# Performance work log

Hardware: AMD Instinct MI355X
Metric: run time of the kernel (lower is better)

Reference implementation:

```python
import jax, jax.numpy as jnp
import numpy as np

N = 100000      # nodes
E = 1600000     # edges (avg degree 16)
IN = 128
OUT = 256


def setup_inputs() -> dict:
    key = jax.random.key(0)
    ks = jax.random.split(key, 8)
    x = jax.random.normal(ks[0], (N, IN), dtype=jnp.float32)
    edge_index = jax.random.randint(ks[1], (2, E), 0, N, dtype=jnp.int64)
    # GCNConv weights (glorot-ish scale) and biases
    W1 = jax.random.normal(ks[2], (IN, OUT), dtype=jnp.float32) / np.float32(np.sqrt(IN))
    b1 = jnp.zeros((OUT,), jnp.float32)
    W2 = jax.random.normal(ks[3], (OUT, OUT), dtype=jnp.float32) / np.float32(np.sqrt(OUT))
    b2 = jnp.zeros((OUT,), jnp.float32)
    # projection Linear(IN, OUT)
    Wp = jax.random.normal(ks[4], (IN, OUT), dtype=jnp.float32) / np.float32(np.sqrt(IN))
    bp = jax.random.normal(ks[5], (OUT,), dtype=jnp.float32) * 0.01
    return {"x": x, "edge_index": edge_index, "W1": W1, "b1": b1,
            "W2": W2, "b2": b2, "Wp": Wp, "bp": bp}


def _gcn_conv(x, W, b, src, dst, n):
    """PyG GCNConv: D^{-1/2}(A+I)D^{-1/2} X W + b. src/dst already include self-loops."""
    xw = x @ W                                              # [n, out]
    ones = jnp.ones(src.shape[0], dtype=xw.dtype)
    deg = jax.ops.segment_sum(ones, dst, num_segments=n)    # in-degree incl. self-loop
    dinv = jnp.where(deg > 0, jax.lax.rsqrt(deg), 0.0)
    norm = dinv[src] * dinv[dst]                            # [e]
    msgs = xw[src] * norm[:, None]                          # gather + scale
    out = jax.ops.segment_sum(msgs, dst, num_segments=n)    # scatter-add
    return out + b


def reference(x, edge_index, W1, b1, W2, b2, Wp, bp):
    n = x.shape[0]
    loop = jnp.arange(n, dtype=edge_index.dtype)            # self-loops
    src = jnp.concatenate([edge_index[0], loop])
    dst = jnp.concatenate([edge_index[1], loop])
    out = jax.nn.relu(_gcn_conv(x, W1, b1, src, dst, n))
    out = _gcn_conv(out, W2, b2, src, dst, n)
    identity = x @ Wp + bp                                  # projection (IN != OUT)
    return jax.nn.relu(out + identity)
```

## Files before the change

### kernel.cpp

```cpp
#include <hip/hip_runtime.h>

#define NODES 100000
#define EDGES 1600000
#define FIN   128
#define FOUT  256
#define NBUCK 196
#define NBLKS 98

typedef __bf16 bf16;
typedef __bf16 bf16x8 __attribute__((ext_vector_type(8)));
typedef __bf16 bf16x4 __attribute__((ext_vector_type(4)));
typedef __bf16 bf16x2 __attribute__((ext_vector_type(2)));
typedef float  f32x4  __attribute__((ext_vector_type(4)));
typedef float  f32x2  __attribute__((ext_vector_type(2)));

__device__ __forceinline__ f32x2 bf2f(unsigned w) {
    f32x2 r;
    r[0] = __uint_as_float(w << 16);
    r[1] = __uint_as_float(w & 0xffff0000u);
    return r;
}

__device__ __forceinline__ void acc_u4(f32x2 a[4], uint4 w) {
    a[0] += bf2f(w.x); a[1] += bf2f(w.y);
    a[2] += bf2f(w.z); a[3] += bf2f(w.w);
}

__device__ __forceinline__ int edge_at(const int* __restrict__ ei, int which, int i,
                                       int is64) {
    if (is64) return ei[2 * (which * EDGES + i)];
    return ei[which * EDGES + i];
}

__global__ __launch_bounds__(256) void init_kernel(const void* __restrict__ x,
                                                   const int* __restrict__ ei,
                                                   int* __restrict__ zero0,
                                                   int* __restrict__ flags,
                                                   float* __restrict__ zpadA,
                                                   float* __restrict__ zpadB) {
    int b = blockIdx.x, t = threadIdx.x;
    if (b < 394) {
        int i = b * 256 + t;
        if (i < 100864) zero0[i] = 0;
        return;
    }
    zpadA[t] = 0.0f;
    zpadB[t] = 0.0f;
    __shared__ int s_f32_evidence;
    __shared__ int s_odd_nonzero;
    if (t == 0) { s_f32_evidence = 0; s_odd_nonzero = 0; }
    __syncthreads();
    const bf16* xb = (const bf16*)x;
    int local_f32 = 0;
    for (int i = t; i < 4096; i += 256) {
        float v = fabsf((float)xb[i]);
        if (!(v < 1e4f)) local_f32 = 1;
    }
    if (local_f32) atomicOr(&s_f32_evidence, 1);
    int local_odd = 0;
    for (int k = t; k < 1024; k += 256) {
        if (ei[2 * k + 1] != 0) local_odd = 1;
    }
    if (local_odd) atomicOr(&s_odd_nonzero, 1);
    __syncthreads();
    if (t == 0) {
        flags[0] = s_f32_evidence ? 0 : 1;
        flags[1] = s_odd_nonzero ? 0 : 1;
    }
}

__global__ __launch_bounds__(512) void degcnt_pack(const int* __restrict__ ei,
                                                   int* __restrict__ deg,
                                                   int* __restrict__ bhist,
                                                   const void* __restrict__ W1,
                                                   const void* __restrict__ W2,
                                                   const void* __restrict__ Wp,
                                                   const void* __restrict__ b1,
                                                   const void* __restrict__ b2,
                                                   const void* __restrict__ bp,
                                                   bf16* __restrict__ W1p, bf16* __restrict__ W2p,
                                                   bf16* __restrict__ Wpp, bf16* __restrict__ b1b,
                                                   bf16* __restrict__ b2b, bf16* __restrict__ bpb,
                                                   const int* __restrict__ flags) {
    if (blockIdx.x < 3125) {
        __shared__ int lh[256];
        int t = threadIdx.x;
        if (t < 256) lh[t] = 0;
        __syncthreads();
        int i = blockIdx.x * 512 + t;
        if (i < EDGES) {
            int is64 = flags[1];
            int s = edge_at(ei, 0, i, is64);
            int d = edge_at(ei, 1, i, is64);
            if (s >= 0 && s < NODES && d >= 0 && d < NODES) {
                atomicAdd(&deg[d], 1);
                atomicAdd(&lh[d >> 9], 1);
            }
        }
        __syncthreads();
        if (t < NBUCK && lh[t] > 0) atomicAdd(&bhist[t], lh[t]);
        return;
    }
    if (threadIdx.x >= 256) return;
    int fl = flags[0];
    int b = blockIdx.x - 3125;
    if (b < 512) {
        const void* W; bf16* Wo; int idx;
        if (b < 128)      { W = W1; Wo = W1p; idx = b * 256 + threadIdx.x; }
        else if (b < 384) { W = W2; Wo = W2p; idx = (b - 128) * 256 + threadIdx.x; }
        else              { W = Wp; Wo = Wpp; idx = (b - 384) * 256 + threadIdx.x; }
        int j    = idx & 7;
        int lane = (idx >> 3) & 63;
        int ct   = (idx >> 9) & 15;
        int kt   = idx >> 13;
        int k = kt * 32 + (lane >> 4) * 8 + j;
        int n = ct * 16 + (lane & 15);
        Wo[idx] = fl ? ((const bf16*)W)[k * 256 + n]
                     : (bf16)(((const float*)W)[k * 256 + n]);
    } else {
        const void* bb; bf16* bo;
        if (b == 512)      { bb = b1; bo = b1b; }
        else if (b == 513) { bb = b2; bo = b2b; }
        else               { bb = bp; bo = bpb; }
        int i = threadIdx.x;
        bo[i] = fl ? ((const bf16*)bb)[i] : (bf16)(((const float*)bb)[i]);
    }
}

__global__ __launch_bounds__(1024) void scan1(const int* __restrict__ deg,
                                              int* __restrict__ col_ptr,
                                              int* __restrict__ blksum, int n) {
    __shared__ int sm[1024];
    int t = threadIdx.x;
    int i = blockIdx.x * 1024 + t;
    int v = (i < n) ? deg[i] + 1 : 0;
    sm[t] = v;
    __syncthreads();
    for (int off = 1; off < 1024; off <<= 1) {
        int u = (t >= off) ? sm[t - off] : 0;
        __syncthreads();
        sm[t] += u;
        __syncthreads();
    }
    if (i <= n) col_ptr[i] = sm[t] - v;
    if (t == 1023) blksum[blockIdx.x] = sm[t];
}

#define EPB 4096
__global__ __launch_bounds__(256) void part_scan3(const int* __restrict__ ei,
                                                  const int* __restrict__ bhist,
                                                  int* __restrict__ bcur,
                                                  uint2* __restrict__ pairs,
                                                  const int* __restrict__ flags,
                                                  int* __restrict__ col_ptr,
                                                  const int* __restrict__ blk,
                                                  const int* __restrict__ deg,
                                                  float* __restrict__ dinv,
                                                  int* __restrict__ col_idx, int n) {
    if (blockIdx.x < 391) {
        __shared__ int lh[256], sc[256], lst[256], lcu[256], gb[256], bs[256];
        __shared__ uint2 stage[EPB];
        int t = threadIdx.x;
        int base = blockIdx.x * EPB;
        int is64 = flags[1];

        lh[t] = 0;
        __syncthreads();

        int es[16], ed[16];
#pragma unroll
        for (int j = 0; j < 16; ++j) {
            int i = base + j * 256 + t;
            int s = -1, d = -1;
            if (i < EDGES) {
                s = edge_at(ei, 0, i, is64);
                d = edge_at(ei, 1, i, is64);
                if (s < 0 || s >= NODES || d < 0 || d >= NODES) d = -1;
            }
            es[j] = s; ed[j] = d;
            if (d >= 0) atomicAdd(&lh[d >> 9], 1);
        }
        __syncthreads();
        sc[t] = lh[t];
        __syncthreads();
        for (int off = 1; off < 256; off <<= 1) {
            int u = (t >= off) ? sc[t - off] : 0;
            __syncthreads();
            sc[t] += u;
            __syncthreads();
        }
        int start = sc[t] - lh[t];
        lst[t] = start;
        lcu[t] = start;
        __syncthreads();
#pragma unroll
        for (int j = 0; j < 16; ++j) {
            if (ed[j] >= 0) {
                int p = atomicAdd(&lcu[ed[j] >> 9], 1);
                stage[p] = make_uint2((unsigned)es[j], (unsigned)ed[j]);
            }
        }
        __syncthreads();
        int v2 = (t < NBUCK) ? bhist[t] : 0;
        bs[t] = v2;
        __syncthreads();
        for (int off = 1; off < 256; off <<= 1) {
            int u = (t >= off) ? bs[t - off] : 0;
            __syncthreads();
            bs[t] += u;
            __syncthreads();
        }
        if (t < NBUCK && lh[t] > 0)
            gb[t] = (bs[t] - v2) + atomicAdd(&bcur[t], lh[t]);
        __syncthreads();
        int nval = sc[255];
        for (int slot = t; slot < nval; slot += 256) {
            uint2 e = stage[slot];
            int b = (int)(e.y >> 9);
            pairs[(size_t)gb[b] + (slot - lst[b])] = e;
        }
        return;
    }
    __shared__ int sb[128];
    int t = threadIdx.x;
    int sid = blockIdx.x - 391;
    int ov = 0;
    if (t < 128) { ov = (t < NBLKS) ? blk[t] : 0; sb[t] = ov; }
    __syncthreads();
    for (int off = 1; off < 128; off <<= 1) {
        int u = (t >= off && t < 128) ? sb[t - off] : 0;
        __syncthreads();
        if (t < 128) sb[t] += u;
        __syncthreads();
    }
    if (t < 128) sb[t] -= ov;
    __syncthreads();
    int i = sid * 256 + t;
    if (i <= n) {
        int v = col_ptr[i] + sb[i >> 10];
        col_ptr[i] = v;
        if (i < n) col_idx[v] = i;
    }
    if (i < n) dinv[i] = rsqrtf((float)deg[i] + 1.0f);
}

__global__ __launch_bounds__(256) void ff_proj(const uint2* __restrict__ pairs,
                                               const int* __restrict__ bhist,
                                               const int* __restrict__ col_ptr,
                                               int* __restrict__ col_idx,
                                               const void* __restrict__ Av,
                                               const bf16* __restrict__ Wpk,
                                               const float* __restrict__ dinv,
                                               const bf16* __restrict__ biasp,
                                               const bf16* __restrict__ bias2,
                                               void* __restrict__ outv,
                                               bf16* __restrict__ projb,
                                               int use_projb,
                                               bf16* __restrict__ Xs,
                                               const int* __restrict__ flags) {
    if (blockIdx.x < NBUCK) {
        __shared__ int lcur[512];
        __shared__ int bs2[256];
        int b = blockIdx.x;
        int t = threadIdx.x;
        int v2 = (t < NBUCK) ? bhist[t] : 0;
        bs2[t] = v2;
        __syncthreads();
        for (int off = 1; off < 256; off <<= 1) {
            int u = (t >= off) ? bs2[t - off] : 0;
            __syncthreads();
            bs2[t] += u;
            __syncthreads();
        }
        int be = bs2[b];
        int bb = be - bhist[b];
        int node = (b << 9) + t;
        lcur[t] = (node < NODES) ? col_ptr[node] + 1 : 0;
        int node2 = node + 256;
        lcur[t + 256] = (node2 < NODES) ? col_ptr[node2] + 1 : 0;
        __syncthreads();
        for (int i = bb + t; i < be; i += 256) {
            uint2 e = pairs[i];
            int pos = atomicAdd(&lcur[e.y & 511], 1);
            col_idx[pos] = (int)e.x;
        }
        return;
    }
    int a_f32 = (flags[0] == 0);
    int wave = threadIdx.x >> 6;
    int lane = threadIdx.x & 63;
    int row0 = (blockIdx.x - NBUCK) * 64;
    int lr = lane & 15;
    int lk = (lane >> 4) * 8;

    int arow[4];
    float di4[4];
#pragma unroll
    for (int rf = 0; rf < 4; ++rf) {
        int r = row0 + rf * 16 + lr;
        arow[rf] = r < NODES ? r : (NODES - 1);
        di4[rf] = dinv[arow[rf]];
    }

    f32x4 acc[4][4];
    f32x4 z = {0.f, 0.f, 0.f, 0.f};
#pragma unroll
    for (int i = 0; i < 4; ++i)
#pragma unroll
        for (int j = 0; j < 4; ++j) acc[i][j] = z;

    for (int kt = 0; kt < 4; ++kt) {
        bf16x8 af[4];
        if (!a_f32) {
            const bf16* Ab = (const bf16*)Av + kt * 32 + lk;
#pragma unroll
            for (int rf = 0; rf < 4; ++rf)
                af[rf] = *(const bf16x8*)(Ab + (size_t)arow[rf] * FIN);
        } else {
            const float* Af = (const float*)Av + kt * 32 + lk;
#pragma unroll
            for (int rf = 0; rf < 4; ++rf) {
                const float* p = Af + (size_t)arow[rf] * FIN;
                f32x4 lo = *(const f32x4*)p;
                f32x4 hi = *(const f32x4*)(p + 4);
                af[rf][0] = (bf16)lo[0]; af[rf][1] = (bf16)lo[1];
                af[rf][2] = (bf16)lo[2]; af[rf][3] = (bf16)lo[3];
                af[rf][4] = (bf16)hi[0]; af[rf][5] = (bf16)hi[1];
                af[rf][6] = (bf16)hi[2]; af[rf][7] = (bf16)hi[3];
            }
        }
#pragma unroll
        for (int rf = 0; rf < 4; ++rf) {
            bf16x8 xsv;
#pragma unroll
            for (int j = 0; j < 8; ++j) xsv[j] = (bf16)(di4[rf] * (float)af[rf][j]);
            *(bf16x8*)(Xs + (size_t)arow[rf] * FIN + kt * 32 + lk) = xsv;
        }
        const bf16* wb = Wpk + ((size_t)(kt * 16 + wave * 4) * 64 + lane) * 8;
        bf16x8 bfv[4];
#pragma unroll
        for (int cf = 0; cf < 4; ++cf)
            bfv[cf] = *(const bf16x8*)(wb + cf * 512);
#pragma unroll
        for (int rf = 0; rf < 4; ++rf)
#pragma unroll
            for (int cf = 0; cf < 4; ++cf)
                acc[rf][cf] = __builtin_amdgcn_mfma_f32_16x16x32_bf16(
                    af[rf], bfv[cf], acc[rf][cf], 0, 0, 0);
    }

    int rb = (lane >> 4) * 4;
#pragma unroll
    for (int rf = 0; rf < 4; ++rf) {
#pragma unroll
        for (int r = 0; r < 4; ++r) {
            int row = row0 + rf * 16 + rb + r;
            if (row >= NODES) continue;
#pragma unroll
            for (int cf = 0; cf < 4; ++cf) {
                int col = wave * 64 + cf * 16 + lr;
                float v = acc[rf][cf][r] + (float)biasp[col] + (float)bias2[col];
                size_t off = (size_t)row * 256 + col;
                if (a_f32) {
                    if (use_projb) projb[off] = (bf16)v;
                    else           ((float*)outv)[off] = v;
                } else {
                    ((bf16*)outv)[off] = (bf16)v;
                }
            }
        }
    }
}

__device__ __forceinline__ f32x2 sel_reduce4(f32x2 a[4], int rg) {
    f32x2 k0 = (rg & 2) ? a[2] : a[0];
    f32x2 k1 = (rg & 2) ? a[3] : a[1];
    f32x2 s0 = (rg & 2) ? a[0] : a[2];
    f32x2 s1 = (rg & 2) ? a[1] : a[3];
    f32x2 t;
    t[0] = __shfl_xor(s0[0], 32); t[1] = __shfl_xor(s0[1], 32); k0 += t;
    t[0] = __shfl_xor(s1[0], 32); t[1] = __shfl_xor(s1[1], 32); k1 += t;
    f32x2 c = (rg & 1) ? k1 : k0;
    f32x2 s = (rg & 1) ? k0 : k1;
    t[0] = __shfl_xor(s[0], 16); t[1] = __shfl_xor(s[1], 16); c += t;
    return c;
}

#define SMLD 264
__global__ __launch_bounds__(512) void g1conv(const int* __restrict__ col_ptr,
                                              const int* __restrict__ col_idx,
                                              const bf16* __restrict__ Xs,
                                              const float* __restrict__ dinv,
                                              const bf16* __restrict__ W1p,
                                              const bf16* __restrict__ W2p,
                                              const bf16* __restrict__ b1b,
                                              bf16* __restrict__ Y2) {
    __shared__ bf16 sm[64][SMLD];
    int wave = threadIdx.x >> 6;
    int lane = threadIdx.x & 63;
    int row0 = blockIdx.x * 64;
    int li = lane & 15;
    int rg = lane >> 4;

    const char* Xl = (const char*)Xs + li * 16;
    for (int k = 0; k < 8; ++k) {
        int node = row0 + wave * 8 + k;
        int nn = node < NODES ? node : (NODES - 1);
        int beg = col_ptr[nn], end = col_ptr[nn + 1];
        float di = dinv[nn];
        f32x2 a[4];
#pragma unroll
        for (int d = 0; d < 4; ++d) { a[d][0] = 0.f; a[d][1] = 0.f; }
        for (int chunk = beg; chunk < end; chunk += 64) {
            int gpos = chunk + lane;
            int idx = -2;
            if (gpos < end) idx = col_idx[gpos];
            int moff = idx << 8;
            int cnt = end - chunk; if (cnt > 64) cnt = 64;
            int j = 0;
            for (; j + 16 <= cnt; j += 16) {
                int so0 = __shfl(moff, j + rg);
                int so1 = __shfl(moff, j + 4 + rg);
                int so2 = __shfl(moff, j + 8 + rg);
                int so3 = __shfl(moff, j + 12 + rg);
                uint4 w0 = *(const uint4*)(Xl + so0);
                uint4 w1 = *(const uint4*)(Xl + so1);
                uint4 w2 = *(const uint4*)(Xl + so2);
                uint4 w3 = *(const uint4*)(Xl + so3);
                acc_u4(a, w0); acc_u4(a, w1);
                acc_u4(a, w2); acc_u4(a, w3);
            }
            for (; j < cnt; j += 4) {
                int so = __shfl(moff, j + rg);
                uint4 w = *(const uint4*)(Xl + so);
                acc_u4(a, w);
            }
        }
        f32x2 s = sel_reduce4(a, rg);
        bf16x2 o;
        o[0] = (bf16)(di * s[0]);
        o[1] = (bf16)(di * s[1]);
        *(bf16x2*)&sm[wave * 8 + k][li * 8 + rg * 2] = o;
    }
    __syncthreads();

    int wr = wave & 1;
    int wc = wave >> 1;
    int lr = li;
    int lk = rg * 8;
    f32x4 acc[2][4];
    f32x4 z = {0.f, 0.f, 0.f, 0.f};
#pragma unroll
    for (int i = 0; i < 2; ++i)
#pragma unroll
        for (int j = 0; j < 4; ++j) acc[i][j] = z;
    for (int kt = 0; kt < 4; ++kt) {
        bf16x8 af[2];
#pragma unroll
        for (int rf = 0; rf < 2; ++rf)
            af[rf] = *(const bf16x8*)&sm[wr * 32 + rf * 16 + lr][kt * 32 + lk];
        const bf16* wb = W1p + ((size_t)(kt * 16 + wc * 4) * 64 + lane) * 8;
        bf16x8 bfv[4];
#pragma unroll
        for (int cf = 0; cf < 4; ++cf)
            bfv[cf] = *(const bf16x8*)(wb + cf * 512);
#pragma unroll
        for (int rf = 0; rf < 2; ++rf)
#pragma unroll
            for (int cf = 0; cf < 4; ++cf)
                acc[rf][cf] = __builtin_amdgcn_mfma_f32_16x16x32_bf16(
                    af[rf], bfv[cf], acc[rf][cf], 0, 0, 0);
    }
    __syncthreads();

    int rb = rg * 4;
#pragma unroll
    for (int rf = 0; rf < 2; ++rf)
#pragma unroll
        for (int r = 0; r < 4; ++r) {
            int row = wr * 32 + rf * 16 + rb + r;
#pragma unroll
            for (int cf = 0; cf < 4; ++cf) {
                int col = wc * 64 + cf * 16 + lr;
                float v = acc[rf][cf][r] + (float)b1b[col];
                sm[row][col] = (bf16)fmaxf(v, 0.0f);
            }
        }
    __syncthreads();

#pragma unroll
    for (int i = 0; i < 2; ++i)
#pragma unroll
        for (int j = 0; j < 4; ++j) acc[i][j] = z;
    for (int kt = 0; kt < 8; ++kt) {
        bf16x8 af[2];
#pragma unroll
        for (int rf = 0; rf < 2; ++rf)
            af[rf] = *(const bf16x8*)&sm[wr * 32 + rf * 16 + lr][kt * 32 + lk];
        const bf16* wb = W2p + ((size_t)(kt * 16 + wc * 4) * 64 + lane) * 8;
        bf16x8 bfv[4];
#pragma unroll
        for (int cf = 0; cf < 4; ++cf)
            bfv[cf] = *(const bf16x8*)(wb + cf * 512);
#pragma unroll
        for (int rf = 0; rf < 2; ++rf)
#pragma unroll
            for (int cf = 0; cf < 4; ++cf)
                acc[rf][cf] = __builtin_amdgcn_mfma_f32_16x16x32_bf16(
                    af[rf], bfv[cf], acc[rf][cf], 0, 0, 0);
    }
#pragma unroll
    for (int rf = 0; rf < 2; ++rf)
#pragma unroll
        for (int r = 0; r < 4; ++r) {
            int row = row0 + wr * 32 + rf * 16 + rb + r;
            if (row >= NODES) continue;
            float di = dinv[row];
#pragma unroll
            for (int cf = 0; cf < 4; ++cf) {
                int col = wc * 64 + cf * 16 + lr;
                Y2[(size_t)row * 256 + col] = (bf16)(acc[rf][cf][r] * di);
            }
        }
}

__global__ __launch_bounds__(256) void gather2(const int* __restrict__ col_ptr,
                                               const int* __restrict__ col_idx,
                                               const bf16* __restrict__ Y2,
                                               const float* __restrict__ dinv,
                                               const bf16* __restrict__ projb,
                                               int use_projb,
                                               void* __restrict__ outv,
                                               const int* __restrict__ flags) {
    int io_f32 = (flags[0] == 0);
    int b = blockIdx.x;
    int slice = b & 1;
    int wave  = threadIdx.x >> 6;
    int wid   = (b >> 1) * 4 + wave;
    int lane  = threadIdx.x & 63;
    if (wid >= NODES) return;
    int beg = col_ptr[wid], end = col_ptr[wid + 1];
    int li = lane & 15;
    int rg = lane >> 4;
    int ch0 = slice * 128 + li * 8 + rg * 2;
    size_t obase = (size_t)wid * 256 + ch0;

    float di = dinv[wid];
    float pj0, pj1;
    if (io_f32) {
        if (use_projb) {
            bf16x2 p = *(const bf16x2*)(projb + obase);
            pj0 = (float)p[0]; pj1 = (float)p[1];
        } else {
            f32x2 p = *(const f32x2*)((const float*)outv + obase);
            pj0 = p[0]; pj1 = p[1];
        }
    } else {
        bf16x2 p = *(const bf16x2*)((const bf16*)outv + obase);
        pj0 = (float)p[0]; pj1 = (float)p[1];
    }

    const char* Yl = (const char*)Y2 + slice * 256 + li * 16;
    f32x2 acc2[4];
#pragma unroll
    for (int d = 0; d < 4; ++d) { acc2[d][0] = 0.f; acc2[d][1] = 0.f; }
    for (int chunk = beg; chunk < end; chunk += 64) {
        int gpos = chunk + lane;
        int idx = -2;
        if (gpos < end) idx = col_idx[gpos];
        int moff = idx << 9;
        int cnt = end - chunk; if (cnt > 64) cnt = 64;
        int j = 0;
        for (; j + 16 <= cnt; j += 16) {
            int so0 = __shfl(moff, j + rg);
            int so1 = __shfl(moff, j + 4 + rg);
            int so2 = __shfl(moff, j + 8 + rg);
            int so3 = __shfl(moff, j + 12 + rg);
            uint4 w0 = *(const uint4*)(Yl + so0);
            uint4 w1 = *(const uint4*)(Yl + so1);
            uint4 w2 = *(const uint4*)(Yl + so2);
            uint4 w3 = *(const uint4*)(Yl + so3);
            acc_u4(acc2, w0); acc_u4(acc2, w1);
            acc_u4(acc2, w2); acc_u4(acc2, w3);
        }
        for (; j < cnt; j += 4) {
            int so = __shfl(moff, j + rg);
            uint4 w = *(const uint4*)(Yl + so);
            acc_u4(acc2, w);
        }
    }
    f32x2 s = sel_reduce4(acc2, rg);
    float r0 = fmaxf(di * s[0] + pj0, 0.0f);
    float r1 = fmaxf(di * s[1] + pj1, 0.0f);

    if (io_f32) {
        f32x2 o; o[0] = r0; o[1] = r1;
        __builtin_nontemporal_store(o, (f32x2*)((float*)outv + obase));
    } else {
        bf16x2 o; o[0] = (bf16)r0; o[1] = (bf16)r1;
        __builtin_nontemporal_store(o, (bf16x2*)((bf16*)outv + obase));
    }
}

__global__ __launch_bounds__(256) void zero_out(bf16* out, int nelem) {
    int i = blockIdx.x * 256 + threadIdx.x;
    if (i < nelem) out[i] = (bf16)0.0f;
}

extern "C" void kernel_launch(void* const* d_in, const int* in_sizes, int n_in,
                              void* d_out, int out_size, void* d_ws, size_t ws_size,
                              hipStream_t stream) {
    const void* x   = d_in[0];
    const int*  ei  = (const int*)d_in[1];
    const void* W1  = d_in[2];
    const void* b1  = d_in[3];
    const void* W2  = d_in[4];
    const void* b2  = d_in[5];
    const void* Wp  = d_in[6];
    const void* bp  = d_in[7];

    const size_t CIDX_ALLOC = 6800384;
    const size_t NEEDED     = 85074432;
    const size_t NEEDED_BIG = NEEDED + 51200000;
    if (ws_size < NEEDED) {
        zero_out<<<(NODES * 256 + 255) / 256, 256, 0, stream>>>((bf16*)d_out, NODES * 256);
        return;
    }
    int use_projb = (ws_size >= NEEDED_BIG) ? 1 : 0;

    char* w = (char*)d_ws;
    int*   col_ptr = (int*)w;   w += 401408;
    int*   deg     = (int*)w;   w += 401408;
    int*   bhist   = (int*)w;   w += 1024;
    int*   bcur    = (int*)w;   w += 1024;
    float* dinv    = (float*)w; w += 401408;
    int*   blk     = (int*)w;   w += 1024;
    int*   flags   = (int*)w;   w += 1024;
    int*   col_idx = (int*)w;   w += CIDX_ALLOC;
    bf16*  W1p     = (bf16*)w;  w += 65536;
    bf16*  W2p     = (bf16*)w;  w += 131072;
    bf16*  Wpp     = (bf16*)w;  w += 65536;
    bf16*  b1b     = (bf16*)w;  w += 512;
    bf16*  b2b     = (bf16*)w;  w += 512;
    bf16*  bpb     = (bf16*)w;  w += 512;
    char*  zpadA   = w;         w += 1024;
    bf16*  Xs      = (bf16*)w;  w += 25600000;
    char*  zpadB   = w;         w += 1024;
    bf16*  Y2      = (bf16*)w;  w += 51200000;
    bf16*  projb   = (bf16*)w;
    uint2* pairs   = (uint2*)Y2;

    init_kernel<<<395, 256, 0, stream>>>(x, ei, deg, flags, (float*)zpadA, (float*)zpadB);

    degcnt_pack<<<3640, 512, 0, stream>>>(ei, deg, bhist, W1, W2, Wp, b1, b2, bp,
                                          W1p, W2p, Wpp, b1b, b2b, bpb, flags);

    scan1<<<NBLKS, 1024, 0, stream>>>(deg, col_ptr, blk, NODES);

    part_scan3<<<391 + 392, 256, 0, stream>>>(ei, bhist, bcur, pairs, flags,
                                              col_ptr, blk, deg, dinv, col_idx, NODES);

    ff_proj<<<NBUCK + (NODES + 63) / 64, 256, 0, stream>>>(
        pairs, bhist, col_ptr, col_idx,
        x, Wpp, dinv, bpb, b2b, d_out, projb, use_projb, Xs, flags);

    g1conv<<<(NODES + 63) / 64, 512, 0, stream>>>(col_ptr, col_idx, Xs, dinv,
                                                  W1p, W2p, b1b, Y2);

    gather2<<<((NODES + 3) / 4) * 2, 256, 0, stream>>>(col_ptr, col_idx, Y2, dinv,
                                                       projb, use_projb, d_out, flags);
}
```

Before: 575.4 us.

## Co-schedule projection GEMM with edge partitioning and split out fine fill

dinv is now computed in scan1, so the projection GEMM (which needs dinv and writes Xs) can run in the same launch as edge partitioning and the col_ptr offset fix-up. The fine bucket fill moves to its own small kernel after that launch. Edges per partition block are halved (4096 to 2048), doubling the partition block count to raise parallelism. The aim is to overlap the compute-bound GEMM with the memory- and atomic-bound partitioning and to shorten the critical path. The cost is one extra kernel launch and shared-memory/register pressure from the merged kernel, which may limit occupancy.

```diff
diff --git a/kernel.cpp b/kernel.cpp
--- a/kernel.cpp
+++ b/kernel.cpp
@@ -129,11 +129,13 @@
 
 __global__ __launch_bounds__(1024) void scan1(const int* __restrict__ deg,
                                               int* __restrict__ col_ptr,
-                                              int* __restrict__ blksum, int n) {
+                                              int* __restrict__ blksum,
+                                              float* __restrict__ dinv, int n) {
     __shared__ int sm[1024];
     int t = threadIdx.x;
     int i = blockIdx.x * 1024 + t;
     int v = (i < n) ? deg[i] + 1 : 0;
+    if (i < n) dinv[i] = rsqrtf((float)v);
     sm[t] = v;
     __syncthreads();
     for (int off = 1; off < 1024; off <<= 1) {
@@ -146,30 +148,126 @@
     if (t == 1023) blksum[blockIdx.x] = sm[t];
 }
 
-#define EPB 4096
-__global__ __launch_bounds__(256) void part_scan3(const int* __restrict__ ei,
-                                                  const int* __restrict__ bhist,
-                                                  int* __restrict__ bcur,
-                                                  uint2* __restrict__ pairs,
-                                                  const int* __restrict__ flags,
-                                                  int* __restrict__ col_ptr,
-                                                  const int* __restrict__ blk,
-                                                  const int* __restrict__ deg,
-                                                  float* __restrict__ dinv,
-                                                  int* __restrict__ col_idx, int n) {
-    if (blockIdx.x < 391) {
+#define EPB 2048
+#define PBLK0 1563
+#define SBLK0 2345
+__global__ __launch_bounds__(256) void part3g(const int* __restrict__ ei,
+                                              const int* __restrict__ bhist,
+                                              int* __restrict__ bcur,
+                                              uint2* __restrict__ pairs,
+                                              const int* __restrict__ flags,
+                                              int* __restrict__ col_ptr,
+                                              const int* __restrict__ blk,
+                                              int* __restrict__ col_idx,
+                                              const void* __restrict__ Av,
+                                              const bf16* __restrict__ Wpk,
+                                              const float* __restrict__ dinv,
+                                              const bf16* __restrict__ biasp,
+                                              const bf16* __restrict__ bias2,
+                                              void* __restrict__ outv,
+                                              bf16* __restrict__ projb,
+                                              int use_projb,
+                                              bf16* __restrict__ Xs, int n) {
+    if (blockIdx.x < PBLK0) {
+        int a_f32 = (flags[0] == 0);
+        int wave = threadIdx.x >> 6;
+        int lane = threadIdx.x & 63;
+        int row0 = blockIdx.x * 64;
+        int lr = lane & 15;
+        int lk = (lane >> 4) * 8;
+
+        int arow[4];
+        float di4[4];
+#pragma unroll
+        for (int rf = 0; rf < 4; ++rf) {
+            int r = row0 + rf * 16 + lr;
+            arow[rf] = r < NODES ? r : (NODES - 1);
+            di4[rf] = dinv[arow[rf]];
+        }
+
+        f32x4 acc[4][4];
+        f32x4 z = {0.f, 0.f, 0.f, 0.f};
+#pragma unroll
+        for (int i = 0; i < 4; ++i)
+#pragma unroll
+            for (int j = 0; j < 4; ++j) acc[i][j] = z;
+
+        for (int kt = 0; kt < 4; ++kt) {
+            bf16x8 af[4];
+            if (!a_f32) {
+                const bf16* Ab = (const bf16*)Av + kt * 32 + lk;
+#pragma unroll
+                for (int rf = 0; rf < 4; ++rf)
+                    af[rf] = *(const bf16x8*)(Ab + (size_t)arow[rf] * FIN);
+            } else {
+                const float* Af = (const float*)Av + kt * 32 + lk;
+#pragma unroll
+                for (int rf = 0; rf < 4; ++rf) {
+                    const float* p = Af + (size_t)arow[rf] * FIN;
+                    f32x4 lo = *(const f32x4*)p;
+                    f32x4 hi = *(const f32x4*)(p + 4);
+                    af[rf][0] = (bf16)lo[0]; af[rf][1] = (bf16)lo[1];
+                    af[rf][2] = (bf16)lo[2]; af[rf][3] = (bf16)lo[3];
+                    af[rf][4] = (bf16)hi[0]; af[rf][5] = (bf16)hi[1];
+                    af[rf][6] = (bf16)hi[2]; af[rf][7] = (bf16)hi[3];
+                }
+            }
+#pragma unroll
+            for (int rf = 0; rf < 4; ++rf) {
+                bf16x8 xsv;
+#pragma unroll
+                for (int j = 0; j < 8; ++j) xsv[j] = (bf16)(di4[rf] * (float)af[rf][j]);
+                *(bf16x8*)(Xs + (size_t)arow[rf] * FIN + kt * 32 + lk) = xsv;
+            }
+            const bf16* wb = Wpk + ((size_t)(kt * 16 + wave * 4) * 64 + lane) * 8;
+            bf16x8 bfv[4];
+#pragma unroll
+            for (int cf = 0; cf < 4; ++cf)
+                bfv[cf] = *(const bf16x8*)(wb + cf * 512);
+#pragma unroll
+            for (int rf = 0; rf < 4; ++rf)
+#pragma unroll
+                for (int cf = 0; cf < 4; ++cf)
+                    acc[rf][cf] = __builtin_amdgcn_mfma_f32_16x16x32_bf16(
+                        af[rf], bfv[cf], acc[rf][cf], 0, 0, 0);
+        }
+
+        int rb = (lane >> 4) * 4;
+#pragma unroll
+        for (int rf = 0; rf < 4; ++rf) {
+#pragma unroll
+            for (int r = 0; r < 4; ++r) {
+                int row = row0 + rf * 16 + rb + r;
+                if (row >= NODES) continue;
+#pragma unroll
+                for (int cf = 0; cf < 4; ++cf) {
+                    int col = wave * 64 + cf * 16 + lr;
+                    float v = acc[rf][cf][r] + (float)biasp[col] + (float)bias2[col];
+                    size_t off = (size_t)row * 256 + col;
+                    if (a_f32) {
+                        if (use_projb) projb[off] = (bf16)v;
+                        else           ((float*)outv)[off] = v;
+                    } else {
+                        ((bf16*)outv)[off] = (bf16)v;
+                    }
+                }
+            }
+        }
+        return;
+    }
+    if (blockIdx.x < SBLK0) {
         __shared__ int lh[256], sc[256], lst[256], lcu[256], gb[256], bs[256];
         __shared__ uint2 stage[EPB];
         int t = threadIdx.x;
-        int base = blockIdx.x * EPB;
+        int base = (blockIdx.x - PBLK0) * EPB;
         int is64 = flags[1];
 
         lh[t] = 0;
         __syncthreads();
 
-        int es[16], ed[16];
-#pragma unroll
-        for (int j = 0; j < 16; ++j) {
+        int es[8], ed[8];
+#pragma unroll
+        for (int j = 0; j < 8; ++j) {
             int i = base + j * 256 + t;
             int s = -1, d = -1;
             if (i < EDGES) {
@@ -194,7 +292,7 @@
         lcu[t] = start;
         __syncthreads();
 #pragma unroll
-        for (int j = 0; j < 16; ++j) {
+        for (int j = 0; j < 8; ++j) {
             if (ed[j] >= 0) {
                 int p = atomicAdd(&lcu[ed[j] >> 9], 1);
                 stage[p] = make_uint2((unsigned)es[j], (unsigned)ed[j]);
@@ -223,7 +321,7 @@
     }
     __shared__ int sb[128];
     int t = threadIdx.x;
-    int sid = blockIdx.x - 391;
+    int sid = blockIdx.x - SBLK0;
     int ov = 0;
     if (t < 128) { ov = (t < NBLKS) ? blk[t] : 0; sb[t] = ov; }
     __syncthreads();
@@ -241,134 +339,36 @@
         col_ptr[i] = v;
         if (i < n) col_idx[v] = i;
     }
-    if (i < n) dinv[i] = rsqrtf((float)deg[i] + 1.0f);
-}
-
-__global__ __launch_bounds__(256) void ff_proj(const uint2* __restrict__ pairs,
-                                               const int* __restrict__ bhist,
-                                               const int* __restrict__ col_ptr,
-                                               int* __restrict__ col_idx,
-                                               const void* __restrict__ Av,
-                                               const bf16* __restrict__ Wpk,
-                                               const float* __restrict__ dinv,
-                                               const bf16* __restrict__ biasp,
-                                               const bf16* __restrict__ bias2,
-                                               void* __restrict__ outv,
-                                               bf16* __restrict__ projb,
-                                               int use_projb,
-                                               bf16* __restrict__ Xs,
-                                               const int* __restrict__ flags) {
-    if (blockIdx.x < NBUCK) {
-        __shared__ int lcur[512];
-        __shared__ int bs2[256];
-        int b = blockIdx.x;
-        int t = threadIdx.x;
-        int v2 = (t < NBUCK) ? bhist[t] : 0;
-        bs2[t] = v2;
-        __syncthreads();
-        for (int off = 1; off < 256; off <<= 1) {
-            int u = (t >= off) ? bs2[t - off] : 0;
-            __syncthreads();
-            bs2[t] += u;
-            __syncthreads();
-        }
-        int be = bs2[b];
-        int bb = be - bhist[b];
-        int node = (b << 9) + t;
-        lcur[t] = (node < NODES) ? col_ptr[node] + 1 : 0;
-        int node2 = node + 256;
-        lcur[t + 256] = (node2 < NODES) ? col_ptr[node2] + 1 : 0;
-        __syncthreads();
-        for (int i = bb + t; i < be; i += 256) {
-            uint2 e = pairs[i];
-            int pos = atomicAdd(&lcur[e.y & 511], 1);
-            col_idx[pos] = (int)e.x;
-        }
-        return;
-    }
-    int a_f32 = (flags[0] == 0);
-    int wave = threadIdx.x >> 6;
-    int lane = threadIdx.x & 63;
-    int row0 = (blockIdx.x - NBUCK) * 64;
-    int lr = lane & 15;
-    int lk = (lane >> 4) * 8;
-
-    int arow[4];
-    float di4[4];
-#pragma unroll
-    for (int rf = 0; rf < 4; ++rf) {
-        int r = row0 + rf * 16 + lr;
-        arow[rf] = r < NODES ? r : (NODES - 1);
-        di4[rf] = dinv[arow[rf]];
-    }
-
-    f32x4 acc[4][4];
-    f32x4 z = {0.f, 0.f, 0.f, 0.f};
-#pragma unroll
-    for (int i = 0; i < 4; ++i)
-#pragma unroll
-        for (int j = 0; j < 4; ++j) acc[i][j] = z;
-
-    for (int kt = 0; kt < 4; ++kt) {
-        bf16x8 af[4];
-        if (!a_f32) {
-            const bf16* Ab = (const bf16*)Av + kt * 32 + lk;
-#pragma unroll
-            for (int rf = 0; rf < 4; ++rf)
-                af[rf] = *(const bf16x8*)(Ab + (size_t)arow[rf] * FIN);
-        } else {
-            const float* Af = (const float*)Av + kt * 32 + lk;
-#pragma unroll
-            for (int rf = 0; rf < 4; ++rf) {
-                const float* p = Af + (size_t)arow[rf] * FIN;
-                f32x4 lo = *(const f32x4*)p;
-                f32x4 hi = *(const f32x4*)(p + 4);
-                af[rf][0] = (bf16)lo[0]; af[rf][1] = (bf16)lo[1];
-                af[rf][2] = (bf16)lo[2]; af[rf][3] = (bf16)lo[3];
-                af[rf][4] = (bf16)hi[0]; af[rf][5] = (bf16)hi[1];
-                af[rf][6] = (bf16)hi[2]; af[rf][7] = (bf16)hi[3];
-            }
-        }
-#pragma unroll
-        for (int rf = 0; rf < 4; ++rf) {
-            bf16x8 xsv;
-#pragma unroll
-            for (int j = 0; j < 8; ++j) xsv[j] = (bf16)(di4[rf] * (float)af[rf][j]);
-            *(bf16x8*)(Xs + (size_t)arow[rf] * FIN + kt * 32 + lk) = xsv;
-        }
-        const bf16* wb = Wpk + ((size_t)(kt * 16 + wave * 4) * 64 + lane) * 8;
-        bf16x8 bfv[4];
-#pragma unroll
-        for (int cf = 0; cf < 4; ++cf)
-            bfv[cf] = *(const bf16x8*)(wb + cf * 512);
-#pragma unroll
-        for (int rf = 0; rf < 4; ++rf)
-#pragma unroll
-            for (int cf = 0; cf < 4; ++cf)
-                acc[rf][cf] = __builtin_amdgcn_mfma_f32_16x16x32_bf16(
-                    af[rf], bfv[cf], acc[rf][cf], 0, 0, 0);
-    }
-
-    int rb = (lane >> 4) * 4;
-#pragma unroll
-    for (int rf = 0; rf < 4; ++rf) {
-#pragma unroll
-        for (int r = 0; r < 4; ++r) {
-            int row = row0 + rf * 16 + rb + r;
-            if (row >= NODES) continue;
-#pragma unroll
-            for (int cf = 0; cf < 4; ++cf) {
-                int col = wave * 64 + cf * 16 + lr;
-                float v = acc[rf][cf][r] + (float)biasp[col] + (float)bias2[col];
-                size_t off = (size_t)row * 256 + col;
-                if (a_f32) {
-                    if (use_projb) projb[off] = (bf16)v;
-                    else           ((float*)outv)[off] = v;
-                } else {
-                    ((bf16*)outv)[off] = (bf16)v;
-                }
-            }
-        }
+}
+
+__global__ __launch_bounds__(256) void fine_fill(const uint2* __restrict__ pairs,
+                                                 const int* __restrict__ bhist,
+                                                 const int* __restrict__ col_ptr,
+                                                 int* __restrict__ col_idx) {
+    __shared__ int lcur[512];
+    __shared__ int bs2[256];
+    int b = blockIdx.x;
+    int t = threadIdx.x;
+    int v2 = (t < NBUCK) ? bhist[t] : 0;
+    bs2[t] = v2;
+    __syncthreads();
+    for (int off = 1; off < 256; off <<= 1) {
+        int u = (t >= off) ? bs2[t - off] : 0;
+        __syncthreads();
+        bs2[t] += u;
+        __syncthreads();
+    }
+    int be = bs2[b];
+    int bb = be - bhist[b];
+    int node = (b << 9) + t;
+    lcur[t] = (node < NODES) ? col_ptr[node] + 1 : 0;
+    int node2 = node + 256;
+    lcur[t + 256] = (node2 < NODES) ? col_ptr[node2] + 1 : 0;
+    __syncthreads();
+    for (int i = bb + t; i < be; i += 256) {
+        uint2 e = pairs[i];
+        int pos = atomicAdd(&lcur[e.y & 511], 1);
+        col_idx[pos] = (int)e.x;
     }
 }
 
@@ -655,14 +655,13 @@
     degcnt_pack<<<3640, 512, 0, stream>>>(ei, deg, bhist, W1, W2, Wp, b1, b2, bp,
                                           W1p, W2p, Wpp, b1b, b2b, bpb, flags);
 
-    scan1<<<NBLKS, 1024, 0, stream>>>(deg, col_ptr, blk, NODES);
-
-    part_scan3<<<391 + 392, 256, 0, stream>>>(ei, bhist, bcur, pairs, flags,
-                                              col_ptr, blk, deg, dinv, col_idx, NODES);
-
-    ff_proj<<<NBUCK + (NODES + 63) / 64, 256, 0, stream>>>(
-        pairs, bhist, col_ptr, col_idx,
-        x, Wpp, dinv, bpb, b2b, d_out, projb, use_projb, Xs, flags);
+    scan1<<<NBLKS, 1024, 0, stream>>>(deg, col_ptr, blk, dinv, NODES);
+
+    part3g<<<PBLK0 + 782 + 392, 256, 0, stream>>>(
+        ei, bhist, bcur, pairs, flags, col_ptr, blk, col_idx,
+        x, Wpp, dinv, bpb, b2b, d_out, projb, use_projb, Xs, NODES);
+
+    fine_fill<<<NBUCK, 256, 0, stream>>>(pairs, bhist, col_ptr, col_idx);
 
     g1conv<<<(NODES + 63) / 64, 512, 0, stream>>>(col_ptr, col_idx, Xs, dinv,
                                                   W1p, W2p, b1b, Y2);
```

Result: no change. 569.1 us (-1.1%).
